# Kernel optimization log

Hardware: AMD Instinct MI355X
Metric: run time of the kernel (lower is better)

## Reference

```python
import jax, jax.numpy as jnp
import numpy as np

COMMITMENT_COST = 0.25


def setup_inputs() -> dict:
    key = jax.random.key(0)
    k1, k2 = jax.random.split(key)
    B, C, H, W = 64, 64, 32, 32
    K = 1024
    inputs = jax.random.normal(k1, (B, C, H, W), dtype=jnp.float32)
    # matches torch init: uniform_(-1/K, 1/K)
    weight = jax.random.uniform(k2, (K, C), dtype=jnp.float32,
                                minval=-1.0 / K, maxval=1.0 / K)
    return {"inputs": inputs, "weight": weight}


def reference(inputs, weight):
    B, C, H, W = inputs.shape
    # (B H W) C
    flat = inputs.transpose(0, 2, 3, 1).reshape(-1, C)
    distances = (jnp.sum(flat * flat, axis=1, keepdims=True)
                 + jnp.sum(weight * weight, axis=1)
                 - 2.0 * (flat @ weight.T))  # [BHW, K]
    encoding_indices = jnp.argmin(distances, axis=1)  # [BHW]
    # one-hot matmul in the original == direct gather
    quantized = jnp.take(weight, encoding_indices, axis=0)  # [BHW, C]
    quantized = quantized.reshape(B, H, W, C).transpose(0, 3, 1, 2)  # B C H W
    e_latent_loss = jnp.mean(
        (jax.lax.stop_gradient(quantized) - inputs) ** 2, axis=(1, 2, 3))
    q_latent_loss = jnp.mean(
        (quantized - jax.lax.stop_gradient(inputs)) ** 2, axis=(1, 2, 3))
    loss = q_latent_loss + COMMITMENT_COST * e_latent_loss  # [B]
    # straight-through estimator
    quantized_st = inputs + jax.lax.stop_gradient(quantized - inputs)
    indices = encoding_indices.reshape(B, H, W)
    return quantized_st, indices, loss
```

## Files before the change

kernel.cpp:

```cpp
#include <hip/hip_runtime.h>
#include <hip/hip_bf16.h>


#define VQ_C    64
#define VQ_K    1024
#define VQ_HW   1024
#define VQ_B    64
#define VQ_ROWS (VQ_B * VQ_HW)
#define BLOCK   256
#define NBLOCKS (VQ_ROWS / BLOCK)
#define NSEG    4
#define SK      (VQ_K / NSEG)

typedef float f32x16 __attribute__((ext_vector_type(16)));

#define XC(c) ((c) < 16 ? x0[(c) & 15] : (c) < 32 ? x1[(c) & 15] \
               : (c) < 48 ? x2[(c) & 15] : x3[(c) & 15])
#define WC(c) ((c) < 16 ? w0[(c) & 15] : (c) < 32 ? w1[(c) & 15] \
               : (c) < 48 ? w2[(c) & 15] : w3[(c) & 15])

__global__ __launch_bounds__(BLOCK) void vq_se2_kernel(
    const float* __restrict__ w, float* __restrict__ se2g) {
    const int k = blockIdx.x * BLOCK + threadIdx.x;
    const float* wr = w + (size_t)k * VQ_C;
    float s0 = 0.f, s1 = 0.f, s2 = 0.f, s3 = 0.f;
    #pragma unroll
    for (int c = 0; c < VQ_C; c += 4) {
        s0 = fmaf(wr[c + 0], wr[c + 0], s0);
        s1 = fmaf(wr[c + 1], wr[c + 1], s1);
        s2 = fmaf(wr[c + 2], wr[c + 2], s2);
        s3 = fmaf(wr[c + 3], wr[c + 3], s3);
    }
    se2g[k] = (s0 + s1) + (s2 + s3);
}

__global__ void
__attribute__((amdgpu_flat_work_group_size(BLOCK, BLOCK), amdgpu_waves_per_eu(4, 4)))
vq_partial(
    const float* __restrict__ inp,
    const float* __restrict__ w,
    const float* __restrict__ se2g,
    float* __restrict__ dist_ws,
    int*   __restrict__ idx_ws)
{
    const int tid = threadIdx.x;
    const int seg = blockIdx.y;
    const int k0  = seg * SK;

    const int r  = blockIdx.x * BLOCK + tid;
    const int b  = r >> 10;
    const int hw = r & (VQ_HW - 1);

    const float* xin = inp + (size_t)b * (VQ_C * VQ_HW) + hw;
    f32x16 x0, x1, x2, x3;
    #pragma unroll
    for (int c = 0; c < 16; ++c) {
        x0[c] = xin[(size_t)(c +  0) * VQ_HW];
        x1[c] = xin[(size_t)(c + 16) * VQ_HW];
        x2[c] = xin[(size_t)(c + 32) * VQ_HW];
        x3[c] = xin[(size_t)(c + 48) * VQ_HW];
    }

    float sx0 = 0.f, sx1 = 0.f, sx2 = 0.f, sx3 = 0.f;
    #pragma unroll
    for (int c = 0; c < VQ_C; c += 4) {
        sx0 = fmaf(XC(c + 0), XC(c + 0), sx0);
        sx1 = fmaf(XC(c + 1), XC(c + 1), sx1);
        sx2 = fmaf(XC(c + 2), XC(c + 2), sx2);
        sx3 = fmaf(XC(c + 3), XC(c + 3), sx3);
    }
    const float sx = (sx0 + sx1) + (sx2 + sx3);

    float best  = 3.402823466e38f;
    int   bestk = k0;
    const float* wp = w + (size_t)k0 * VQ_C;
    const float* sp = se2g + k0;

    #pragma unroll 1
    for (int k = 0; k < SK; ++k, wp += VQ_C, ++sp) {
        f32x16 w0, w1, w2, w3;
        float  se2k;
        asm volatile(
            "s_load_dwordx16 %0, %5, 0x0\n\t"
            "s_load_dwordx16 %1, %5, 0x40\n\t"
            "s_load_dwordx16 %2, %5, 0x80\n\t"
            "s_load_dwordx16 %3, %5, 0xc0\n\t"
            "s_load_dword    %4, %6, 0x0\n\t"
            "s_waitcnt lgkmcnt(0)"
            : "=&s"(w0), "=&s"(w1), "=&s"(w2), "=&s"(w3), "=&s"(se2k)
            : "s"(wp), "s"(sp));

        float d0 = 0.f, d1 = 0.f, d2 = 0.f, d3 = 0.f;
        #pragma unroll
        for (int c = 0; c < VQ_C; c += 4) {
            d0 = fmaf(WC(c + 0), XC(c + 0), d0);
            d1 = fmaf(WC(c + 1), XC(c + 1), d1);
            d2 = fmaf(WC(c + 2), XC(c + 2), d2);
            d3 = fmaf(WC(c + 3), XC(c + 3), d3);
        }
        const float dot = (d0 + d1) + (d2 + d3);
        const float d = (sx + se2k) - 2.f * dot;
        if (d < best) { best = d; bestk = k0 + k; }
    }

    dist_ws[(size_t)seg * VQ_ROWS + r] = best;
    idx_ws [(size_t)seg * VQ_ROWS + r] = bestk;
}

__global__ __launch_bounds__(BLOCK) void vq_finalize_kernel(
    const float* __restrict__ inp,
    const float* __restrict__ w,
    const float* __restrict__ dist_ws,
    const int*   __restrict__ idx_ws,
    float* __restrict__ out_q,
    float* __restrict__ out_idx,
    float* __restrict__ partials,
    int nseg)
{
    __shared__ float red[BLOCK];
    const int tid = threadIdx.x;
    const int r   = blockIdx.x * BLOCK + tid;
    const int b   = r >> 10;
    const int hw  = r & (VQ_HW - 1);

    float best  = dist_ws[r];
    int   bestk = idx_ws[r];
    for (int s = 1; s < nseg; ++s) {
        const float d  = dist_ws[(size_t)s * VQ_ROWS + r];
        const int   kk = idx_ws [(size_t)s * VQ_ROWS + r];
        if (d < best) { best = d; bestk = kk; }
    }

    const float* xin  = inp + (size_t)b * (VQ_C * VQ_HW) + hw;
    const float* q    = w + (size_t)bestk * VQ_C;
    float*       outr = out_q + (size_t)b * (VQ_C * VQ_HW) + hw;

    float sd0 = 0.f, sd1 = 0.f, sd2 = 0.f, sd3 = 0.f;
    #pragma unroll
    for (int c = 0; c < VQ_C; c += 4) {
        float x0 = xin[(size_t)(c + 0) * VQ_HW];
        float x1 = xin[(size_t)(c + 1) * VQ_HW];
        float x2 = xin[(size_t)(c + 2) * VQ_HW];
        float x3 = xin[(size_t)(c + 3) * VQ_HW];
        float q0 = q[c + 0], q1 = q[c + 1], q2 = q[c + 2], q3 = q[c + 3];
        outr[(size_t)(c + 0) * VQ_HW] = x0 + (q0 - x0);
        outr[(size_t)(c + 1) * VQ_HW] = x1 + (q1 - x1);
        outr[(size_t)(c + 2) * VQ_HW] = x2 + (q2 - x2);
        outr[(size_t)(c + 3) * VQ_HW] = x3 + (q3 - x3);
        float e0 = q0 - x0, e1 = q1 - x1, e2 = q2 - x2, e3 = q3 - x3;
        sd0 = fmaf(e0, e0, sd0);
        sd1 = fmaf(e1, e1, sd1);
        sd2 = fmaf(e2, e2, sd2);
        sd3 = fmaf(e3, e3, sd3);
    }
    out_idx[r] = (float)bestk;

    red[tid] = (sd0 + sd1) + (sd2 + sd3);
    __syncthreads();
    #pragma unroll
    for (int s = BLOCK / 2; s > 0; s >>= 1) {
        if (tid < s) red[tid] += red[tid + s];
        __syncthreads();
    }
    if (tid == 0) partials[blockIdx.x] = red[0];
}

__global__ __launch_bounds__(64) void vq_loss_kernel(
    const float* __restrict__ partials,
    float* __restrict__ loss)
{
    const int b = threadIdx.x;
    const float s = (partials[4 * b + 0] + partials[4 * b + 1])
                  + (partials[4 * b + 2] + partials[4 * b + 3]);
    const float L = s * (1.0f / 65536.0f);
    loss[b] = L + 0.25f * L;
}

__global__ __launch_bounds__(BLOCK) void vq_main_kernel(
    const float* __restrict__ inp,
    const float* __restrict__ w,
    float* __restrict__ out_q,
    float* __restrict__ out_idx,
    float* __restrict__ partials)
{
    __shared__ float se2s[VQ_K];
    __shared__ float red[BLOCK];
    const int tid = threadIdx.x;

    for (int k = tid; k < VQ_K; k += BLOCK) {
        const float* wr = w + k * VQ_C;
        float s0 = 0.f, s1 = 0.f, s2 = 0.f, s3 = 0.f;
        #pragma unroll
        for (int c = 0; c < VQ_C; c += 4) {
            s0 = fmaf(wr[c + 0], wr[c + 0], s0);
            s1 = fmaf(wr[c + 1], wr[c + 1], s1);
            s2 = fmaf(wr[c + 2], wr[c + 2], s2);
            s3 = fmaf(wr[c + 3], wr[c + 3], s3);
        }
        se2s[k] = (s0 + s1) + (s2 + s3);
    }
    __syncthreads();

    const int r  = blockIdx.x * BLOCK + tid;
    const int b  = r >> 10;
    const int hw = r & (VQ_HW - 1);

    const float* xin = inp + (size_t)b * (VQ_C * VQ_HW) + hw;
    float x[VQ_C];
    #pragma unroll
    for (int c = 0; c < VQ_C; ++c) x[c] = xin[(size_t)c * VQ_HW];

    float sx0 = 0.f, sx1 = 0.f, sx2 = 0.f, sx3 = 0.f;
    #pragma unroll
    for (int c = 0; c < VQ_C; c += 4) {
        sx0 = fmaf(x[c + 0], x[c + 0], sx0);
        sx1 = fmaf(x[c + 1], x[c + 1], sx1);
        sx2 = fmaf(x[c + 2], x[c + 2], sx2);
        sx3 = fmaf(x[c + 3], x[c + 3], sx3);
    }
    const float sx = (sx0 + sx1) + (sx2 + sx3);

    float best = 3.402823466e38f;
    int bestk = 0;
    for (int k = 0; k < VQ_K; ++k) {
        const float* wr = w + (size_t)k * VQ_C;
        float d0 = 0.f, d1 = 0.f, d2 = 0.f, d3 = 0.f;
        #pragma unroll
        for (int c = 0; c < VQ_C; c += 4) {
            d0 = fmaf(wr[c + 0], x[c + 0], d0);
            d1 = fmaf(wr[c + 1], x[c + 1], d1);
            d2 = fmaf(wr[c + 2], x[c + 2], d2);
            d3 = fmaf(wr[c + 3], x[c + 3], d3);
        }
        const float dot = (d0 + d1) + (d2 + d3);
        const float d = (sx + se2s[k]) - 2.f * dot;
        if (d < best) { best = d; bestk = k; }
    }

    const float* q = w + (size_t)bestk * VQ_C;
    float* outr = out_q + (size_t)b * (VQ_C * VQ_HW) + hw;
    float sd0 = 0.f, sd1 = 0.f, sd2 = 0.f, sd3 = 0.f;
    #pragma unroll
    for (int c = 0; c < VQ_C; c += 4) {
        float q0 = q[c + 0], q1 = q[c + 1], q2 = q[c + 2], q3 = q[c + 3];
        float x0 = x[c + 0], x1 = x[c + 1], x2 = x[c + 2], x3 = x[c + 3];
        outr[(size_t)(c + 0) * VQ_HW] = x0 + (q0 - x0);
        outr[(size_t)(c + 1) * VQ_HW] = x1 + (q1 - x1);
        outr[(size_t)(c + 2) * VQ_HW] = x2 + (q2 - x2);
        outr[(size_t)(c + 3) * VQ_HW] = x3 + (q3 - x3);
        float e0 = q0 - x0, e1 = q1 - x1, e2 = q2 - x2, e3 = q3 - x3;
        sd0 = fmaf(e0, e0, sd0);
        sd1 = fmaf(e1, e1, sd1);
        sd2 = fmaf(e2, e2, sd2);
        sd3 = fmaf(e3, e3, sd3);
    }
    out_idx[r] = (float)bestk;

    red[tid] = (sd0 + sd1) + (sd2 + sd3);
    __syncthreads();
    #pragma unroll
    for (int s = BLOCK / 2; s > 0; s >>= 1) {
        if (tid < s) red[tid] += red[tid + s];
        __syncthreads();
    }
    if (tid == 0) partials[blockIdx.x] = red[0];
}

extern "C" void kernel_launch(void* const* d_in, const int* in_sizes, int n_in,
                              void* d_out, int out_size, void* d_ws, size_t ws_size,
                              hipStream_t stream) {
    const float* inp = (const float*)d_in[0];
    const float* w   = (const float*)d_in[1];

    float* out_q    = (float*)d_out;
    float* out_idx  = (float*)d_out + 4194304;
    float* out_loss = (float*)d_out + 4194304 + 65536;

    const size_t se2_f   = VQ_K;
    const size_t dist_f  = (size_t)NSEG * VQ_ROWS;
    const size_t idx_f   = (size_t)NSEG * VQ_ROWS;
    const size_t part_f  = NBLOCKS;
    const size_t need    = (se2_f + dist_f + idx_f + part_f) * 4;

    if (ws_size >= need) {
        float* se2g     = (float*)d_ws;
        float* dist_ws  = se2g + se2_f;
        int*   idx_ws   = (int*)(dist_ws + dist_f);
        float* partials = (float*)(idx_ws + idx_f);

        vq_se2_kernel<<<VQ_K / BLOCK, BLOCK, 0, stream>>>(w, se2g);
        vq_partial<<<dim3(NBLOCKS, NSEG), BLOCK, 0, stream>>>(inp, w, se2g, dist_ws, idx_ws);
        vq_finalize_kernel<<<NBLOCKS, BLOCK, 0, stream>>>(inp, w, dist_ws, idx_ws,
                                                          out_q, out_idx, partials, NSEG);
        vq_loss_kernel<<<1, 64, 0, stream>>>(partials, out_loss);
    } else {
        float* partials = (float*)d_ws;
        vq_main_kernel<<<NBLOCKS, BLOCK, 0, stream>>>(inp, w, out_q, out_idx, partials);
        vq_loss_kernel<<<1, 64, 0, stream>>>(partials, out_loss);
    }
}
```

Baseline: 128.0 us.

## Stagger per-wave codebook start offsets and split codebook into eight segments

Each wave now begins its scan of the codebook segment at a different rotated offset, chosen from its wave id and block index, and wraps around to the start. The goal is to spread scalar-cache traffic across codebook rows instead of every wave fetching the same row at once. When the workspace is large enough, the codebook is also split into 8 segments instead of 4, giving more blocks with shorter loops at the cost of more partial results for the finalize kernel to merge. Tie-breaking now prefers the lower index so argmin results stay the same despite the rotated order.

```diff
diff --git a/kernel.cpp b/kernel.cpp
--- a/kernel.cpp
+++ b/kernel.cpp
@@ -9,8 +9,6 @@
 #define VQ_ROWS (VQ_B * VQ_HW)
 #define BLOCK   256
 #define NBLOCKS (VQ_ROWS / BLOCK)
-#define NSEG    4
-#define SK      (VQ_K / NSEG)
 
 typedef float f32x16 __attribute__((ext_vector_type(16)));
 
@@ -18,6 +16,34 @@
                : (c) < 48 ? x2[(c) & 15] : x3[(c) & 15])
 #define WC(c) ((c) < 16 ? w0[(c) & 15] : (c) < 32 ? w1[(c) & 15] \
                : (c) < 48 ? w2[(c) & 15] : w3[(c) & 15])
+
+#define KSTEP(KABS)                                                       \
+    do {                                                                  \
+        f32x16 w0, w1, w2, w3;                                            \
+        float  se2k;                                                      \
+        asm volatile(                                                     \
+            "s_load_dwordx16 %0, %5, 0x0\n\t"                             \
+            "s_load_dwordx16 %1, %5, 0x40\n\t"                            \
+            "s_load_dwordx16 %2, %5, 0x80\n\t"                            \
+            "s_load_dwordx16 %3, %5, 0xc0\n\t"                            \
+            "s_load_dword    %4, %6, 0x0\n\t"                             \
+            "s_waitcnt lgkmcnt(0)"                                        \
+            : "=&s"(w0), "=&s"(w1), "=&s"(w2), "=&s"(w3), "=&s"(se2k)     \
+            : "s"(wp), "s"(sp));                                          \
+        float d0 = 0.f, d1 = 0.f, d2 = 0.f, d3 = 0.f;                     \
+        _Pragma("unroll")                                                 \
+        for (int c = 0; c < VQ_C; c += 4) {                               \
+            d0 = fmaf(WC(c + 0), XC(c + 0), d0);                          \
+            d1 = fmaf(WC(c + 1), XC(c + 1), d1);                          \
+            d2 = fmaf(WC(c + 2), XC(c + 2), d2);                          \
+            d3 = fmaf(WC(c + 3), XC(c + 3), d3);                          \
+        }                                                                 \
+        const float dot = (d0 + d1) + (d2 + d3);                          \
+        const float d = (sx + se2k) - 2.f * dot;                          \
+        if (d < best || (d == best && (KABS) < bestk)) {                  \
+            best = d; bestk = (KABS);                                     \
+        }                                                                 \
+    } while (0)
 
 __global__ __launch_bounds__(BLOCK) void vq_se2_kernel(
     const float* __restrict__ w, float* __restrict__ se2g) {
@@ -34,6 +60,7 @@
     se2g[k] = (s0 + s1) + (s2 + s3);
 }
 
+template <int SK>
 __global__ void
 __attribute__((amdgpu_flat_work_group_size(BLOCK, BLOCK), amdgpu_waves_per_eu(4, 4)))
 vq_partial(
@@ -71,36 +98,24 @@
     }
     const float sx = (sx0 + sx1) + (sx2 + sx3);
 
+    const int wave  = __builtin_amdgcn_readfirstlane(tid >> 6);
+    const int phase = ((wave * (SK / 4)) + ((blockIdx.x & 3) * (SK / 16)))
+                      & (SK - 1);
+
     float best  = 3.402823466e38f;
     int   bestk = k0;
-    const float* wp = w + (size_t)k0 * VQ_C;
-    const float* sp = se2g + k0;
-
+
+    const float* wp = w + (size_t)(k0 + phase) * VQ_C;
+    const float* sp = se2g + k0 + phase;
     #pragma unroll 1
-    for (int k = 0; k < SK; ++k, wp += VQ_C, ++sp) {
-        f32x16 w0, w1, w2, w3;
-        float  se2k;
-        asm volatile(
-            "s_load_dwordx16 %0, %5, 0x0\n\t"
-            "s_load_dwordx16 %1, %5, 0x40\n\t"
-            "s_load_dwordx16 %2, %5, 0x80\n\t"
-            "s_load_dwordx16 %3, %5, 0xc0\n\t"
-            "s_load_dword    %4, %6, 0x0\n\t"
-            "s_waitcnt lgkmcnt(0)"
-            : "=&s"(w0), "=&s"(w1), "=&s"(w2), "=&s"(w3), "=&s"(se2k)
-            : "s"(wp), "s"(sp));
-
-        float d0 = 0.f, d1 = 0.f, d2 = 0.f, d3 = 0.f;
-        #pragma unroll
-        for (int c = 0; c < VQ_C; c += 4) {
-            d0 = fmaf(WC(c + 0), XC(c + 0), d0);
-            d1 = fmaf(WC(c + 1), XC(c + 1), d1);
-            d2 = fmaf(WC(c + 2), XC(c + 2), d2);
-            d3 = fmaf(WC(c + 3), XC(c + 3), d3);
-        }
-        const float dot = (d0 + d1) + (d2 + d3);
-        const float d = (sx + se2k) - 2.f * dot;
-        if (d < best) { best = d; bestk = k0 + k; }
+    for (int k = phase; k < SK; ++k, wp += VQ_C, ++sp) {
+        KSTEP(k0 + k);
+    }
+    wp = w + (size_t)k0 * VQ_C;
+    sp = se2g + k0;
+    #pragma unroll 1
+    for (int k = 0; k < phase; ++k, wp += VQ_C, ++sp) {
+        KSTEP(k0 + k);
     }
 
     dist_ws[(size_t)seg * VQ_ROWS + r] = best;
@@ -128,7 +143,7 @@
     for (int s = 1; s < nseg; ++s) {
         const float d  = dist_ws[(size_t)s * VQ_ROWS + r];
         const int   kk = idx_ws [(size_t)s * VQ_ROWS + r];
-        if (d < best) { best = d; bestk = kk; }
+        if (d < best || (d == best && kk < bestk)) { best = d; bestk = kk; }
     }
 
     const float* xin  = inp + (size_t)b * (VQ_C * VQ_HW) + hw;
@@ -276,22 +291,32 @@
     float* out_idx  = (float*)d_out + 4194304;
     float* out_loss = (float*)d_out + 4194304 + 65536;
 
-    const size_t se2_f   = VQ_K;
-    const size_t dist_f  = (size_t)NSEG * VQ_ROWS;
-    const size_t idx_f   = (size_t)NSEG * VQ_ROWS;
-    const size_t part_f  = NBLOCKS;
-    const size_t need    = (se2_f + dist_f + idx_f + part_f) * 4;
-
-    if (ws_size >= need) {
+    const size_t se2_f  = VQ_K;
+    const size_t part_f = NBLOCKS;
+    auto need = [&](int ns) {
+        return (se2_f + (size_t)ns * VQ_ROWS * 2 + part_f) * 4;
+    };
+
+    int nseg = 0;
+    if (ws_size >= need(8))      nseg = 8;
+    else if (ws_size >= need(4)) nseg = 4;
+
+    if (nseg > 0) {
         float* se2g     = (float*)d_ws;
         float* dist_ws  = se2g + se2_f;
-        int*   idx_ws   = (int*)(dist_ws + dist_f);
-        float* partials = (float*)(idx_ws + idx_f);
+        int*   idx_ws   = (int*)(dist_ws + (size_t)nseg * VQ_ROWS);
+        float* partials = (float*)((int*)idx_ws + (size_t)nseg * VQ_ROWS);
 
         vq_se2_kernel<<<VQ_K / BLOCK, BLOCK, 0, stream>>>(w, se2g);
-        vq_partial<<<dim3(NBLOCKS, NSEG), BLOCK, 0, stream>>>(inp, w, se2g, dist_ws, idx_ws);
+        if (nseg == 8) {
+            vq_partial<VQ_K / 8><<<dim3(NBLOCKS, 8), BLOCK, 0, stream>>>(
+                inp, w, se2g, dist_ws, idx_ws);
+        } else {
+            vq_partial<VQ_K / 4><<<dim3(NBLOCKS, 4), BLOCK, 0, stream>>>(
+                inp, w, se2g, dist_ws, idx_ws);
+        }
         vq_finalize_kernel<<<NBLOCKS, BLOCK, 0, stream>>>(inp, w, dist_ws, idx_ws,
-                                                          out_q, out_idx, partials, NSEG);
+                                                          out_q, out_idx, partials, nseg);
         vq_loss_kernel<<<1, 64, 0, stream>>>(partials, out_loss);
     } else {
         float* partials = (float*)d_ws;
```

After: 144.3 us. 1.13x slower.
